# Performance work log

Measured on AMD Instinct MI355X. Metric: run time of the kernel, lower is better.

## Reference

```python
import jax, jax.numpy as jnp
import numpy as np

N, S, T, D = 8, 2048, 2048, 1024


def setup_inputs() -> dict:
    key0 = jax.random.key(0)
    ks = jax.random.split(key0, 6)
    scale = 1.0 / np.sqrt(D).astype(np.float32)
    query = jax.random.normal(ks[0], (N, S, D), dtype=jnp.float32)
    key = jax.random.normal(ks[1], (N, T, D), dtype=jnp.float32)
    value = jax.random.normal(ks[2], (N, T, D), dtype=jnp.float32)
    # nn.Linear(D, D, bias=False) weights, shape [out, in]
    Wq = jax.random.normal(ks[3], (D, D), dtype=jnp.float32) * scale
    Wk = jax.random.normal(ks[4], (D, D), dtype=jnp.float32) * scale
    Wv = jax.random.normal(ks[5], (D, D), dtype=jnp.float32) * scale
    # causal mask: 1 on/below diagonal, 0 above (zeros become -inf additively)
    attn_mask = jnp.tril(jnp.ones((S, T), dtype=jnp.float32))
    return {"key": key, "query": query, "value": value,
            "Wq": Wq, "Wk": Wk, "Wv": Wv, "attn_mask": attn_mask}


def reference(key, query, value, Wq, Wk, Wv, attn_mask):
    d = query.shape[-1]
    q = query @ Wq.T              # [N,S,D]
    k = key @ Wk.T                # [N,T,D]
    v = value @ Wv.T              # [N,T,D]
    scores = jnp.einsum('nsd,ntd->nst', q, k)          # [N,S,T]
    # masked_fill(mask==0, -inf) then ADD the (nonzero) mask values
    additive = jnp.where(attn_mask == 0, -jnp.inf, attn_mask)
    scores = scores + additive                          # broadcast [S,T] -> [N,S,T]
    # NOTE: torch code divides by D**(-0.5), i.e. multiplies by sqrt(D). Faithful.
    attn = jax.nn.softmax(scores * jnp.sqrt(jnp.float32(d)), axis=-1)
    return jnp.einsum('nst,ntd->nsd', attn, v)          # [N,S,D]
```

## Files before the change

kernel.cpp:

```cpp
#include <hip/hip_runtime.h>
#include <hip/hip_bf16.h>


typedef __attribute__((ext_vector_type(4))) float f32x4;
typedef __attribute__((ext_vector_type(8))) short bf16x8;
typedef __attribute__((ext_vector_type(4))) short s16x4;

#define DEVI __device__ __forceinline__

DEVI unsigned short f2bf(float x) {
  union { float f; unsigned u; } v; v.f = x;
  unsigned r = v.u + 0x7FFFu + ((v.u >> 16) & 1u);
  return (unsigned short)(r >> 16);
}
DEVI float bf2f(unsigned short b) {
  union { float f; unsigned u; } v; v.u = ((unsigned)b) << 16;
  return v.f;
}

DEVI void gload16(const void* g, void* l) {
#if __has_builtin(__builtin_amdgcn_global_load_lds)
  typedef __attribute__((address_space(1))) const unsigned int* gas_u32;
  typedef __attribute__((address_space(3))) unsigned int* las_u32;
  __builtin_amdgcn_global_load_lds(
      (gas_u32)(unsigned long long)g,
      (las_u32)(unsigned int)(unsigned long long)l, 16, 0, 0);
#else
  *(bf16x8*)l = *(const bf16x8*)g;
#endif
}

DEVI int xcd_swizzle(int bid, int nwg) {
  if (nwg & 7) return bid;
  int cpx = nwg >> 3;
  return (bid & 7) * cpx + (bid >> 3);
}

DEVI void stage_pair(const unsigned short* __restrict__ s0, long long rs0,
                     const unsigned short* __restrict__ s1, long long rs1,
                     short* lds, int tid) {
#pragma unroll
  for (int it = 0; it < 4; ++it) {
    int ii = it * 256 + tid;
    int r = ii >> 3;
    int c8 = (ii & 7) ^ (r & 7);
    const unsigned short* src = (c8 < 4)
        ? s0 + (long long)r * rs0 + (c8 & 3) * 8
        : s1 + (long long)r * rs1 + (c8 & 3) * 8;
    gload16(src, &lds[ii * 8]);
  }
}

constexpr int NB = 8, SS = 2048, TT = 2048, DD = 1024;
constexpr long long TILE_E = 16384;

__global__ __launch_bounds__(256) void split_hl_k(
    const float* __restrict__ in, unsigned short* __restrict__ hi,
    unsigned short* __restrict__ lo, long long n4)
{
  long long i = (long long)blockIdx.x * 256 + threadIdx.x;
  long long stride = (long long)gridDim.x * 256;
  for (; i < n4; i += stride) {
    f32x4 v = ((const f32x4*)in)[i];
    s16x4 h, l;
#pragma unroll
    for (int e = 0; e < 4; ++e) {
      unsigned short hh = f2bf(v[e]);
      h[e] = (short)hh;
      l[e] = (short)f2bf(v[e] - bf2f(hh));
    }
    ((s16x4*)hi)[i] = h;
    ((s16x4*)lo)[i] = l;
  }
}

__global__ __launch_bounds__(256) void split_h_k(
    const float* __restrict__ in, unsigned short* __restrict__ hi, long long n4)
{
  long long i = (long long)blockIdx.x * 256 + threadIdx.x;
  long long stride = (long long)gridDim.x * 256;
  for (; i < n4; i += stride) {
    f32x4 v = ((const f32x4*)in)[i];
    s16x4 h;
#pragma unroll
    for (int e = 0; e < 4; ++e) h[e] = (short)f2bf(v[e]);
    ((s16x4*)hi)[i] = h;
  }
}

template<int NMFMA, bool SPLIT_OUT>
__global__ __launch_bounds__(256, 2) void gemm_bt(
    const unsigned short* __restrict__ Ah_g, const unsigned short* __restrict__ Al_g,
    const unsigned short* __restrict__ Bh_g, const unsigned short* __restrict__ Bl_g,
    unsigned short* __restrict__ Chi, unsigned short* __restrict__ Clo,
    int Nn, int K,
    long long aStride, long long bStride, long long cStride,
    int tilesM, int tilesN)
{
  constexpr int NBUF = (NMFMA == 3) ? 4 : 2;
  __shared__ short lds[NBUF * 8192];

  int tid = threadIdx.x;
  int lane = tid & 63, wid = tid >> 6;
  int wr = wid >> 1, wc = wid & 1;
  int l15 = lane & 15, lq = lane >> 4;

  int wg = xcd_swizzle(blockIdx.x, gridDim.x);
  int tilesPer = tilesM * tilesN;
  int b = wg / tilesPer;
  int rem = wg % tilesPer;
  int mt = rem / tilesN, nt = rem % tilesN;

  const unsigned short* Agh = Ah_g + (long long)b * aStride + (long long)mt * 128 * K;
  const unsigned short* Bgh = Bh_g + (long long)b * bStride + (long long)nt * 128 * K;
  const unsigned short* Agl = (NMFMA == 3) ? Al_g + (long long)b * aStride + (long long)mt * 128 * K : nullptr;
  const unsigned short* Bgl = (NMFMA == 3) ? Bl_g + (long long)b * bStride + (long long)nt * 128 * K : nullptr;

  f32x4 acc[4][4];
#pragma unroll
  for (int i = 0; i < 4; ++i)
#pragma unroll
    for (int j = 0; j < 4; ++j) acc[i][j] = (f32x4){0.f, 0.f, 0.f, 0.f};

  auto stage = [&](int t, int half) {
    int k0 = t * 32;
    if constexpr (NMFMA == 3) {
      stage_pair(Agh + k0, K, Agl + k0, K, lds + half * 16384, tid);
      stage_pair(Bgh + k0, K, Bgl + k0, K, lds + half * 16384 + 8192, tid);
    } else {
      stage_pair(Agh + k0, K, Bgh + k0, K, lds + half * 8192, tid);
    }
  };

  auto compute = [&](int half) {
    if constexpr (NMFMA == 3) {
      const short* U = lds + half * 16384;
      const short* Vb2 = U + 8192;
      bf16x8 afh[4], afl[4], bfh[4], bfl[4];
#pragma unroll
      for (int i = 0; i < 4; ++i) {
        int ra = wr * 64 + i * 16 + l15;
        int sa = (ra & 7) << 4;
        afh[i] = *(const bf16x8*)(&U[((ra * 128 + lq * 16) ^ sa) >> 1]);
        afl[i] = *(const bf16x8*)(&U[((ra * 128 + 64 + lq * 16) ^ sa) >> 1]);
        int rb = wc * 64 + i * 16 + l15;
        int sb = (rb & 7) << 4;
        bfh[i] = *(const bf16x8*)(&Vb2[((rb * 128 + lq * 16) ^ sb) >> 1]);
        bfl[i] = *(const bf16x8*)(&Vb2[((rb * 128 + 64 + lq * 16) ^ sb) >> 1]);
      }
#pragma unroll
      for (int i = 0; i < 4; ++i)
#pragma unroll
        for (int j = 0; j < 4; ++j) {
          acc[i][j] = __builtin_amdgcn_mfma_f32_16x16x32_bf16(afh[i], bfh[j], acc[i][j], 0, 0, 0);
          acc[i][j] = __builtin_amdgcn_mfma_f32_16x16x32_bf16(afh[i], bfl[j], acc[i][j], 0, 0, 0);
          acc[i][j] = __builtin_amdgcn_mfma_f32_16x16x32_bf16(afl[i], bfh[j], acc[i][j], 0, 0, 0);
        }
    } else {
      const short* W = lds + half * 8192;
      bf16x8 af[4], bfr[4];
#pragma unroll
      for (int i = 0; i < 4; ++i) {
        int ra = wr * 64 + i * 16 + l15;
        af[i] = *(const bf16x8*)(&W[((ra * 128 + lq * 16) ^ ((ra & 7) << 4)) >> 1]);
        int rb = wc * 64 + i * 16 + l15;
        bfr[i] = *(const bf16x8*)(&W[((rb * 128 + 64 + lq * 16) ^ ((rb & 7) << 4)) >> 1]);
      }
#pragma unroll
      for (int i = 0; i < 4; ++i)
#pragma unroll
        for (int j = 0; j < 4; ++j)
          acc[i][j] = __builtin_amdgcn_mfma_f32_16x16x32_bf16(af[i], bfr[j], acc[i][j], 0, 0, 0);
    }
  };

  int NT = K >> 5;
  stage(0, 0);
  __syncthreads();
  for (int t = 0; t < NT; t += 2) {
    if (t + 1 < NT) stage(t + 1, 1);
    compute(0);
    __syncthreads();
    if (t + 2 < NT) stage(t + 2, 0);
    compute(1);
    __syncthreads();
  }

  unsigned short* ch = Chi + (long long)b * cStride;
  unsigned short* cl = SPLIT_OUT ? (Clo + (long long)b * cStride) : nullptr;
#pragma unroll
  for (int i = 0; i < 4; ++i)
#pragma unroll
    for (int j = 0; j < 4; ++j)
#pragma unroll
      for (int e = 0; e < 4; ++e) {
        int row = mt * 128 + wr * 64 + i * 16 + lq * 4 + e;
        int col = nt * 128 + wc * 64 + j * 16 + l15;
        float vv = acc[i][j][e];
        unsigned short h = f2bf(vv);
        ch[(long long)row * Nn + col] = h;
        if constexpr (SPLIT_OUT) cl[(long long)row * Nn + col] = f2bf(vv - bf2f(h));
      }
}

__global__ __launch_bounds__(256, 2) void qk_bt(
    const unsigned short* __restrict__ qh, const unsigned short* __restrict__ ql,
    const unsigned short* __restrict__ kh, const unsigned short* __restrict__ kl,
    float* __restrict__ Sg)
{
  __shared__ short lds[4 * 8192];

  int tid = threadIdx.x;
  int lane = tid & 63, wid = tid >> 6;
  int wr = wid >> 1, wc = wid & 1;
  int l15 = lane & 15, lq = lane >> 4;

  int wg = xcd_swizzle(blockIdx.x, gridDim.x);
  int b = wg / 136;
  int idx = wg % 136;
  int st = (int)((sqrtf(8.f * (float)idx + 1.f) - 1.f) * 0.5f);
  while ((st + 1) * (st + 2) / 2 <= idx) ++st;
  while (st * (st + 1) / 2 > idx) --st;
  int tt = idx - st * (st + 1) / 2;

  const unsigned short* Agh = qh + (long long)b * SS * DD + (long long)st * 128 * DD;
  const unsigned short* Agl = ql + (long long)b * SS * DD + (long long)st * 128 * DD;
  const unsigned short* Bgh = kh + (long long)b * TT * DD + (long long)tt * 128 * DD;
  const unsigned short* Bgl = kl + (long long)b * TT * DD + (long long)tt * 128 * DD;

  f32x4 acc[4][4];
#pragma unroll
  for (int i = 0; i < 4; ++i)
#pragma unroll
    for (int j = 0; j < 4; ++j) acc[i][j] = (f32x4){0.f, 0.f, 0.f, 0.f};

  auto stage = [&](int t, int half) {
    int k0 = t * 32;
    stage_pair(Agh + k0, DD, Agl + k0, DD, lds + half * 16384, tid);
    stage_pair(Bgh + k0, DD, Bgl + k0, DD, lds + half * 16384 + 8192, tid);
  };
  auto compute = [&](int half) {
    const short* U = lds + half * 16384;
    const short* Vb2 = U + 8192;
    bf16x8 afh[4], afl[4], bfh[4], bfl[4];
#pragma unroll
    for (int i = 0; i < 4; ++i) {
      int ra = wr * 64 + i * 16 + l15;
      int sa = (ra & 7) << 4;
      afh[i] = *(const bf16x8*)(&U[((ra * 128 + lq * 16) ^ sa) >> 1]);
      afl[i] = *(const bf16x8*)(&U[((ra * 128 + 64 + lq * 16) ^ sa) >> 1]);
      int rb = wc * 64 + i * 16 + l15;
      int sb = (rb & 7) << 4;
      bfh[i] = *(const bf16x8*)(&Vb2[((rb * 128 + lq * 16) ^ sb) >> 1]);
      bfl[i] = *(const bf16x8*)(&Vb2[((rb * 128 + 64 + lq * 16) ^ sb) >> 1]);
    }
#pragma unroll
    for (int i = 0; i < 4; ++i)
#pragma unroll
      for (int j = 0; j < 4; ++j) {
        acc[i][j] = __builtin_amdgcn_mfma_f32_16x16x32_bf16(afh[i], bfh[j], acc[i][j], 0, 0, 0);
        acc[i][j] = __builtin_amdgcn_mfma_f32_16x16x32_bf16(afh[i], bfl[j], acc[i][j], 0, 0, 0);
        acc[i][j] = __builtin_amdgcn_mfma_f32_16x16x32_bf16(afl[i], bfh[j], acc[i][j], 0, 0, 0);
      }
  };

  stage(0, 0);
  __syncthreads();
  for (int t = 0; t < 32; t += 2) {
    if (t + 1 < 32) stage(t + 1, 1);
    compute(0);
    __syncthreads();
    if (t + 2 < 32) stage(t + 2, 0);
    compute(1);
    __syncthreads();
  }

  float* Sb = Sg + ((long long)b * 136 + idx) * TILE_E;
#pragma unroll
  for (int i = 0; i < 4; ++i)
#pragma unroll
    for (int j = 0; j < 4; ++j)
#pragma unroll
      for (int e = 0; e < 4; ++e) {
        int row = wr * 64 + i * 16 + lq * 4 + e;
        int col = wc * 64 + j * 16 + l15;
        Sb[(long long)row * 128 + col] = acc[i][j][e];
      }
}

__global__ __launch_bounds__(256) void softmax_kernel(float* __restrict__ Sg)
{
  __shared__ float red[8];
  int blk = blockIdx.x;
  int b = blk >> 11, s = blk & 2047;
  int st = s >> 7, r = s & 127;
  long long tri = (long long)st * (st + 1) / 2;
  const float* tb = Sg + ((long long)b * 136 + tri) * TILE_E + (long long)r * 128;

  int tid = threadIdx.x;
  int lane = tid & 63, wid = tid >> 6;

  int c0 = tid * 8;
  int tt = c0 >> 7, cc = c0 & 127;
  bool live = (c0 <= s);
  f32x4 v0 = {0.f, 0.f, 0.f, 0.f}, v1 = {0.f, 0.f, 0.f, 0.f};
  if (live) {
    const float* seg = tb + (long long)tt * TILE_E + cc;
    v0 = *(const f32x4*)seg;
    v1 = *(const f32x4*)(seg + 4);
  }

  float m = -3.0e38f;
#pragma unroll
  for (int e = 0; e < 4; ++e) {
    if (c0 + e <= s) m = fmaxf(m, v0[e]);
    if (c0 + 4 + e <= s) m = fmaxf(m, v1[e]);
  }
#pragma unroll
  for (int o = 32; o > 0; o >>= 1) m = fmaxf(m, __shfl_xor(m, o));
  if (lane == 0) red[wid] = m;
  __syncthreads();
  m = fmaxf(fmaxf(red[0], red[1]), fmaxf(red[2], red[3]));

  const float C = 46.16624130844683f;
  float p0[4], p1[4];
  float sum = 0.f;
#pragma unroll
  for (int e = 0; e < 4; ++e) {
    p0[e] = (c0 + e <= s) ? exp2f((v0[e] - m) * C) : 0.f;
    sum += p0[e];
    p1[e] = (c0 + 4 + e <= s) ? exp2f((v1[e] - m) * C) : 0.f;
    sum += p1[e];
  }
#pragma unroll
  for (int o = 32; o > 0; o >>= 1) sum += __shfl_xor(sum, o);
  if (lane == 0) red[4 + wid] = sum;
  __syncthreads();
  float inv = 1.f / (red[4] + red[5] + red[6] + red[7]);

  union { bf16x8 v; s16x4 h[2]; } w;
#pragma unroll
  for (int e = 0; e < 4; ++e) {
    w.h[0][e] = (short)f2bf(p0[e] * inv);
    w.h[1][e] = (short)f2bf(p1[e] * inv);
  }
  __syncthreads();
  if (c0 < (st + 1) * 128) {
    unsigned short* pw = (unsigned short*)Sg +
        (((long long)b * 136 + tri + tt) * TILE_E) * 2 + (long long)r * 256 + cc;
    *(bf16x8*)pw = w.v;
  }
}

__global__ __launch_bounds__(256, 2) void pv_bt(
    const unsigned short* __restrict__ P, const unsigned short* __restrict__ vT,
    float* __restrict__ Out)
{
  __shared__ short lds[2 * 8192];

  int tid = threadIdx.x;
  int lane = tid & 63, wid = tid >> 6;
  int wr = wid >> 1, wc = wid & 1;
  int l15 = lane & 15, lq = lane >> 4;

  int wg = xcd_swizzle(blockIdx.x, gridDim.x);
  int b = wg >> 7;
  int rem = wg & 127;
  int st = rem >> 3, dt = rem & 7;

  const unsigned short* Ps = P + ((long long)b * 136 + (long long)st * (st + 1) / 2) * (TILE_E * 2);
  const unsigned short* Vb = vT + (long long)b * DD * TT + (long long)dt * 128 * TT;
  int NT = (st + 1) * 4;

  f32x4 acc[4][4];
#pragma unroll
  for (int i = 0; i < 4; ++i)
#pragma unroll
    for (int j = 0; j < 4; ++j) acc[i][j] = (f32x4){0.f, 0.f, 0.f, 0.f};

  auto stage = [&](int t, int half) {
    int t0 = t * 32;
    const unsigned short* s0 = Ps + (long long)(t0 >> 7) * (TILE_E * 2) + (t0 & 127);
    stage_pair(s0, 256, Vb + t0, TT, lds + half * 8192, tid);
  };
  auto compute = [&](int half) {
    const short* W = lds + half * 8192;
    bf16x8 af[4], bfr[4];
#pragma unroll
    for (int i = 0; i < 4; ++i) {
      int ra = wr * 64 + i * 16 + l15;
      af[i] = *(const bf16x8*)(&W[((ra * 128 + lq * 16) ^ ((ra & 7) << 4)) >> 1]);
      int rb = wc * 64 + i * 16 + l15;
      bfr[i] = *(const bf16x8*)(&W[((rb * 128 + 64 + lq * 16) ^ ((rb & 7) << 4)) >> 1]);
    }
#pragma unroll
    for (int i = 0; i < 4; ++i)
#pragma unroll
      for (int j = 0; j < 4; ++j)
        acc[i][j] = __builtin_amdgcn_mfma_f32_16x16x32_bf16(af[i], bfr[j], acc[i][j], 0, 0, 0);
  };

  stage(0, 0);
  __syncthreads();
  for (int t = 0; t < NT; t += 2) {
    if (t + 1 < NT) stage(t + 1, 1);
    compute(0);
    __syncthreads();
    if (t + 2 < NT) stage(t + 2, 0);
    compute(1);
    __syncthreads();
  }

  float* Ob = Out + (long long)b * SS * DD;
#pragma unroll
  for (int i = 0; i < 4; ++i)
#pragma unroll
    for (int j = 0; j < 4; ++j)
#pragma unroll
      for (int e = 0; e < 4; ++e) {
        int row = st * 128 + wr * 64 + i * 16 + lq * 4 + e;
        int col = dt * 128 + wc * 64 + j * 16 + l15;
        Ob[(long long)row * DD + col] = acc[i][j][e];
      }
}

extern "C" void kernel_launch(void* const* d_in, const int* in_sizes, int n_in,
                              void* d_out, int out_size, void* d_ws, size_t ws_size,
                              hipStream_t stream) {
  (void)in_sizes; (void)n_in; (void)out_size;
  const float* key   = (const float*)d_in[0];
  const float* query = (const float*)d_in[1];
  const float* value = (const float*)d_in[2];
  const float* Wq    = (const float*)d_in[3];
  const float* Wk    = (const float*)d_in[4];
  const float* Wv    = (const float*)d_in[5];
  float* Out = (float*)d_out;

  const long long SD = (long long)SS * DD;
  const long long DT = (long long)DD * TT;
  const long long WN = (long long)DD * DD;

  const unsigned long long PLANE_B  = (unsigned long long)SD * 2;
  const unsigned long long WPLANE_B = (unsigned long long)WN * 2;
  const unsigned long long SCORE_B  = 136ull * TILE_E * 4;

  auto need = [&](int g) -> unsigned long long {
    return 5ull * WPLANE_B + (unsigned long long)g * (SCORE_B + 5ull * PLANE_B);
  };
  int G = 1;
  for (int g : {8, 4, 2, 1}) if (ws_size >= need(g)) { G = g; break; }

  char* ws = (char*)d_ws;
  size_t off = 0;
  auto alloc = [&](unsigned long long bytes) { char* p = ws + off; off += bytes; return p; };

  unsigned short* wqh = (unsigned short*)alloc(WPLANE_B);
  unsigned short* wql = (unsigned short*)alloc(WPLANE_B);
  unsigned short* wkh = (unsigned short*)alloc(WPLANE_B);
  unsigned short* wkl = (unsigned short*)alloc(WPLANE_B);
  unsigned short* wvh = (unsigned short*)alloc(WPLANE_B);
  char* slab = alloc((unsigned long long)G * SCORE_B);
  unsigned short* qh  = (unsigned short*)alloc((unsigned long long)G * PLANE_B);
  unsigned short* ql  = (unsigned short*)alloc((unsigned long long)G * PLANE_B);
  unsigned short* kh  = (unsigned short*)alloc((unsigned long long)G * PLANE_B);
  unsigned short* kl  = (unsigned short*)alloc((unsigned long long)G * PLANE_B);
  unsigned short* vT  = (unsigned short*)alloc((unsigned long long)G * PLANE_B);

  unsigned short* iah = (unsigned short*)slab;
  unsigned short* ial = (unsigned short*)(slab + (unsigned long long)G * PLANE_B);
  float* Sg = (float*)slab;

  split_hl_k<<<512, 256, 0, stream>>>(Wq, wqh, wql, WN / 4);
  split_hl_k<<<512, 256, 0, stream>>>(Wk, wkh, wkl, WN / 4);
  split_h_k<<<512, 256, 0, stream>>>(Wv, wvh, WN / 4);

  for (int b0 = 0; b0 < NB; b0 += G) {
    long long n4 = (long long)G * SD / 4;
    split_hl_k<<<2048, 256, 0, stream>>>(query + (long long)b0 * SD, iah, ial, n4);
    gemm_bt<3, true><<<G * 128, 256, 0, stream>>>(
        iah, ial, wqh, wql, qh, ql, DD, DD, SD, 0, SD, 16, 8);
    split_hl_k<<<2048, 256, 0, stream>>>(key + (long long)b0 * SD, iah, ial, n4);
    gemm_bt<3, true><<<G * 128, 256, 0, stream>>>(
        iah, ial, wkh, wkl, kh, kl, DD, DD, SD, 0, SD, 16, 8);
    split_h_k<<<2048, 256, 0, stream>>>(value + (long long)b0 * SD, iah, n4);
    gemm_bt<1, false><<<G * 128, 256, 0, stream>>>(
        wvh, nullptr, iah, nullptr, vT, nullptr, TT, DD, 0, SD, DT, 8, 16);
    qk_bt<<<G * 136, 256, 0, stream>>>(qh, ql, kh, kl, Sg);
    softmax_kernel<<<G * SS, 256, 0, stream>>>(Sg);
    pv_bt<<<G * 128, 256, 0, stream>>>(
        (const unsigned short*)Sg, vT, Out + (long long)b0 * SD);
  }
}
```

Baseline: 530.0 us.

## Retile causal QK^T kernel to 64x128 tiles with two-wave blocks and single buffer

The QK^T kernel now uses 64-row by 128-column tiles computed by 128-thread blocks (two waves), doubling the grid to 272 tiles per batch with a new triangular index mapping over half-height row strips. Staging becomes single-buffered with inline swizzled global-to-LDS loads, and MFMA sections are bracketed with s_setprio. The aim is more blocks and occupancy to fill CUs and better load balance on the causal triangle. In exchange it loses the double-buffered overlap of loads and compute and gets less operand reuse per tile.

```diff
diff --git a/kernel.cpp b/kernel.cpp
--- a/kernel.cpp
+++ b/kernel.cpp
@@ -203,30 +203,30 @@
       }
 }
 
-__global__ __launch_bounds__(256, 2) void qk_bt(
+__global__ __launch_bounds__(128, 3) void qk_bt(
     const unsigned short* __restrict__ qh, const unsigned short* __restrict__ ql,
     const unsigned short* __restrict__ kh, const unsigned short* __restrict__ kl,
     float* __restrict__ Sg)
 {
-  __shared__ short lds[4 * 8192];
+  __shared__ short lds[12288];
+  short* Ab = lds;
+  short* Bb = lds + 4096;
 
   int tid = threadIdx.x;
   int lane = tid & 63, wid = tid >> 6;
-  int wr = wid >> 1, wc = wid & 1;
   int l15 = lane & 15, lq = lane >> 4;
 
   int wg = xcd_swizzle(blockIdx.x, gridDim.x);
-  int b = wg / 136;
-  int idx = wg % 136;
-  int st = (int)((sqrtf(8.f * (float)idx + 1.f) - 1.f) * 0.5f);
-  while ((st + 1) * (st + 2) / 2 <= idx) ++st;
-  while (st * (st + 1) / 2 > idx) --st;
-  int tt = idx - st * (st + 1) / 2;
-
-  const unsigned short* Agh = qh + (long long)b * SS * DD + (long long)st * 128 * DD;
-  const unsigned short* Agl = ql + (long long)b * SS * DD + (long long)st * 128 * DD;
-  const unsigned short* Bgh = kh + (long long)b * TT * DD + (long long)tt * 128 * DD;
-  const unsigned short* Bgl = kl + (long long)b * TT * DD + (long long)tt * 128 * DD;
+  int b = wg / 272;
+  int idx = wg % 272;
+  int st = 0, cum = 0;
+  while (cum + (st >> 1) + 1 <= idx) { cum += (st >> 1) + 1; ++st; }
+  int tc = idx - cum;
+
+  const unsigned short* Agh = qh + (long long)b * SS * DD + (long long)st * 64 * DD;
+  const unsigned short* Agl = ql + (long long)b * SS * DD + (long long)st * 64 * DD;
+  const unsigned short* Bgh = kh + (long long)b * TT * DD + (long long)tc * 128 * DD;
+  const unsigned short* Bgl = kl + (long long)b * TT * DD + (long long)tc * 128 * DD;
 
   f32x4 acc[4][4];
 #pragma unroll
@@ -234,25 +234,43 @@
 #pragma unroll
     for (int j = 0; j < 4; ++j) acc[i][j] = (f32x4){0.f, 0.f, 0.f, 0.f};
 
-  auto stage = [&](int t, int half) {
+  for (int t = 0; t < 32; ++t) {
     int k0 = t * 32;
-    stage_pair(Agh + k0, DD, Agl + k0, DD, lds + half * 16384, tid);
-    stage_pair(Bgh + k0, DD, Bgl + k0, DD, lds + half * 16384 + 8192, tid);
-  };
-  auto compute = [&](int half) {
-    const short* U = lds + half * 16384;
-    const short* Vb2 = U + 8192;
+    __syncthreads();
+#pragma unroll
+    for (int it = 0; it < 4; ++it) {
+      int ii = it * 128 + tid;
+      int r = ii >> 3;
+      int c8 = (ii & 7) ^ (r & 7);
+      const unsigned short* src = (c8 < 4)
+          ? Agh + (long long)r * DD + k0 + (c8 & 3) * 8
+          : Agl + (long long)r * DD + k0 + (c8 & 3) * 8;
+      gload16(src, &Ab[ii * 8]);
+    }
+#pragma unroll
+    for (int it = 0; it < 8; ++it) {
+      int ii = it * 128 + tid;
+      int r = ii >> 3;
+      int c8 = (ii & 7) ^ (r & 7);
+      const unsigned short* src = (c8 < 4)
+          ? Bgh + (long long)r * DD + k0 + (c8 & 3) * 8
+          : Bgl + (long long)r * DD + k0 + (c8 & 3) * 8;
+      gload16(src, &Bb[ii * 8]);
+    }
+    __syncthreads();
+
+    __builtin_amdgcn_s_setprio(1);
     bf16x8 afh[4], afl[4], bfh[4], bfl[4];
 #pragma unroll
     for (int i = 0; i < 4; ++i) {
-      int ra = wr * 64 + i * 16 + l15;
+      int ra = i * 16 + l15;
       int sa = (ra & 7) << 4;
-      afh[i] = *(const bf16x8*)(&U[((ra * 128 + lq * 16) ^ sa) >> 1]);
-      afl[i] = *(const bf16x8*)(&U[((ra * 128 + 64 + lq * 16) ^ sa) >> 1]);
-      int rb = wc * 64 + i * 16 + l15;
+      afh[i] = *(const bf16x8*)(&Ab[((ra * 128 + lq * 16) ^ sa) >> 1]);
+      afl[i] = *(const bf16x8*)(&Ab[((ra * 128 + 64 + lq * 16) ^ sa) >> 1]);
+      int rb = wid * 64 + i * 16 + l15;
       int sb = (rb & 7) << 4;
-      bfh[i] = *(const bf16x8*)(&Vb2[((rb * 128 + lq * 16) ^ sb) >> 1]);
-      bfl[i] = *(const bf16x8*)(&Vb2[((rb * 128 + 64 + lq * 16) ^ sb) >> 1]);
+      bfh[i] = *(const bf16x8*)(&Bb[((rb * 128 + lq * 16) ^ sb) >> 1]);
+      bfl[i] = *(const bf16x8*)(&Bb[((rb * 128 + 64 + lq * 16) ^ sb) >> 1]);
     }
 #pragma unroll
     for (int i = 0; i < 4; ++i)
@@ -262,28 +280,20 @@
         acc[i][j] = __builtin_amdgcn_mfma_f32_16x16x32_bf16(afh[i], bfl[j], acc[i][j], 0, 0, 0);
         acc[i][j] = __builtin_amdgcn_mfma_f32_16x16x32_bf16(afl[i], bfh[j], acc[i][j], 0, 0, 0);
       }
-  };
-
-  stage(0, 0);
-  __syncthreads();
-  for (int t = 0; t < 32; t += 2) {
-    if (t + 1 < 32) stage(t + 1, 1);
-    compute(0);
-    __syncthreads();
-    if (t + 2 < 32) stage(t + 2, 0);
-    compute(1);
-    __syncthreads();
-  }
-
-  float* Sb = Sg + ((long long)b * 136 + idx) * TILE_E;
+    __builtin_amdgcn_s_setprio(0);
+  }
+
+  int st128 = st >> 1;
+  long long ptile = (long long)b * 136 + (long long)st128 * (st128 + 1) / 2 + tc;
+  float* Sb = Sg + ptile * TILE_E + (long long)(st & 1) * 64 * 128;
 #pragma unroll
   for (int i = 0; i < 4; ++i)
 #pragma unroll
     for (int j = 0; j < 4; ++j)
 #pragma unroll
       for (int e = 0; e < 4; ++e) {
-        int row = wr * 64 + i * 16 + lq * 4 + e;
-        int col = wc * 64 + j * 16 + l15;
+        int row = i * 16 + lq * 4 + e;
+        int col = wid * 64 + j * 16 + l15;
         Sb[(long long)row * 128 + col] = acc[i][j][e];
       }
 }
@@ -485,7 +495,7 @@
     split_h_k<<<2048, 256, 0, stream>>>(value + (long long)b0 * SD, iah, n4);
     gemm_bt<1, false><<<G * 128, 256, 0, stream>>>(
         wvh, nullptr, iah, nullptr, vT, nullptr, TT, DD, 0, SD, DT, 8, 16);
-    qk_bt<<<G * 136, 256, 0, stream>>>(qh, ql, kh, kl, Sg);
+    qk_bt<<<G * 272, 128, 0, stream>>>(qh, ql, kh, kl, Sg);
     softmax_kernel<<<G * SS, 256, 0, stream>>>(Sg);
     pv_bt<<<G * 128, 256, 0, stream>>>(
         (const unsigned short*)Sg, vT, Out + (long long)b0 * SD);
```

Measured after the change: 655.1 us. +23.6%, slower.

## Prefetch two stages ahead with vmcnt waits, persistent two-tile GEMM, reverse PV order

Applied to the files above, without the earlier changes.

Replaces the double-buffered __syncthreads loop with a scheme that issues two stages up front, waits on vmcnt counts plus a raw barrier, and refills the buffer just consumed. This keeps one global load in flight during each compute step. Compute sections run at raised wave priority. The projection GEMM now processes two M tiles per workgroup with half the grid, and the PV kernel schedules long causal rows first for better load balance. The hand-written waitcnt values depend on the exact number of loads per stage, which makes them fragile.

```diff
diff --git a/kernel.cpp b/kernel.cpp
--- a/kernel.cpp
+++ b/kernel.cpp
@@ -36,6 +36,9 @@
   return (bid & 7) * cpx + (bid >> 3);
 }
 
+#define WAITBAR(N) asm volatile("s_waitcnt vmcnt(" #N ")\ns_barrier" ::: "memory")
+#define BAR()      asm volatile("s_barrier" ::: "memory")
+
 DEVI void stage_pair(const unsigned short* __restrict__ s0, long long rs0,
                      const unsigned short* __restrict__ s1, long long rs1,
                      short* lds, int tid) {
@@ -97,8 +100,8 @@
     long long aStride, long long bStride, long long cStride,
     int tilesM, int tilesN)
 {
-  constexpr int NBUF = (NMFMA == 3) ? 4 : 2;
-  __shared__ short lds[NBUF * 8192];
+  constexpr int HALF = (NMFMA == 3) ? 16384 : 8192;
+  __shared__ short lds[2 * HALF];
 
   int tid = threadIdx.x;
   int lane = tid & 63, wid = tid >> 6;
@@ -106,101 +109,110 @@
   int l15 = lane & 15, lq = lane >> 4;
 
   int wg = xcd_swizzle(blockIdx.x, gridDim.x);
-  int tilesPer = tilesM * tilesN;
+  int tilesM2 = tilesM >> 1;
+  int tilesPer = tilesM2 * tilesN;
   int b = wg / tilesPer;
   int rem = wg % tilesPer;
-  int mt = rem / tilesN, nt = rem % tilesN;
-
-  const unsigned short* Agh = Ah_g + (long long)b * aStride + (long long)mt * 128 * K;
+  int mt2 = rem / tilesN, nt = rem % tilesN;
+
   const unsigned short* Bgh = Bh_g + (long long)b * bStride + (long long)nt * 128 * K;
-  const unsigned short* Agl = (NMFMA == 3) ? Al_g + (long long)b * aStride + (long long)mt * 128 * K : nullptr;
   const unsigned short* Bgl = (NMFMA == 3) ? Bl_g + (long long)b * bStride + (long long)nt * 128 * K : nullptr;
 
-  f32x4 acc[4][4];
-#pragma unroll
-  for (int i = 0; i < 4; ++i)
-#pragma unroll
-    for (int j = 0; j < 4; ++j) acc[i][j] = (f32x4){0.f, 0.f, 0.f, 0.f};
-
-  auto stage = [&](int t, int half) {
-    int k0 = t * 32;
-    if constexpr (NMFMA == 3) {
-      stage_pair(Agh + k0, K, Agl + k0, K, lds + half * 16384, tid);
-      stage_pair(Bgh + k0, K, Bgl + k0, K, lds + half * 16384 + 8192, tid);
-    } else {
-      stage_pair(Agh + k0, K, Bgh + k0, K, lds + half * 8192, tid);
+  for (int hm = 0; hm < 2; ++hm) {
+    int mt = mt2 + hm * tilesM2;
+    const unsigned short* Agh = Ah_g + (long long)b * aStride + (long long)mt * 128 * K;
+    const unsigned short* Agl = (NMFMA == 3) ? Al_g + (long long)b * aStride + (long long)mt * 128 * K : nullptr;
+
+    f32x4 acc[4][4];
+#pragma unroll
+    for (int i = 0; i < 4; ++i)
+#pragma unroll
+      for (int j = 0; j < 4; ++j) acc[i][j] = (f32x4){0.f, 0.f, 0.f, 0.f};
+
+    auto stage = [&](int t, int h) {
+      int k0 = t * 32;
+      if constexpr (NMFMA == 3) {
+        stage_pair(Agh + k0, K, Agl + k0, K, lds + h * HALF, tid);
+        stage_pair(Bgh + k0, K, Bgl + k0, K, lds + h * HALF + 8192, tid);
+      } else {
+        stage_pair(Agh + k0, K, Bgh + k0, K, lds + h * HALF, tid);
+      }
+    };
+    auto compute = [&](int h) {
+      __builtin_amdgcn_s_setprio(1);
+      if constexpr (NMFMA == 3) {
+        const short* U = lds + h * HALF;
+        const short* V = U + 8192;
+        bf16x8 afh[4], afl[4], bfh[4], bfl[4];
+#pragma unroll
+        for (int i = 0; i < 4; ++i) {
+          int ra = wr * 64 + i * 16 + l15;
+          int sa = (ra & 7) << 4;
+          afh[i] = *(const bf16x8*)(&U[((ra * 128 + lq * 16) ^ sa) >> 1]);
+          afl[i] = *(const bf16x8*)(&U[((ra * 128 + 64 + lq * 16) ^ sa) >> 1]);
+          int rb = wc * 64 + i * 16 + l15;
+          int sb = (rb & 7) << 4;
+          bfh[i] = *(const bf16x8*)(&V[((rb * 128 + lq * 16) ^ sb) >> 1]);
+          bfl[i] = *(const bf16x8*)(&V[((rb * 128 + 64 + lq * 16) ^ sb) >> 1]);
+        }
+#pragma unroll
+        for (int i = 0; i < 4; ++i)
+#pragma unroll
+          for (int j = 0; j < 4; ++j) {
+            acc[i][j] = __builtin_amdgcn_mfma_f32_16x16x32_bf16(afh[i], bfh[j], acc[i][j], 0, 0, 0);
+            acc[i][j] = __builtin_amdgcn_mfma_f32_16x16x32_bf16(afh[i], bfl[j], acc[i][j], 0, 0, 0);
+            acc[i][j] = __builtin_amdgcn_mfma_f32_16x16x32_bf16(afl[i], bfh[j], acc[i][j], 0, 0, 0);
+          }
+      } else {
+        const short* W = lds + h * HALF;
+        bf16x8 af[4], bfr[4];
+#pragma unroll
+        for (int i = 0; i < 4; ++i) {
+          int ra = wr * 64 + i * 16 + l15;
+          af[i] = *(const bf16x8*)(&W[((ra * 128 + lq * 16) ^ ((ra & 7) << 4)) >> 1]);
+          int rb = wc * 64 + i * 16 + l15;
+          bfr[i] = *(const bf16x8*)(&W[((rb * 128 + 64 + lq * 16) ^ ((rb & 7) << 4)) >> 1]);
+        }
+#pragma unroll
+        for (int i = 0; i < 4; ++i)
+#pragma unroll
+          for (int j = 0; j < 4; ++j)
+            acc[i][j] = __builtin_amdgcn_mfma_f32_16x16x32_bf16(af[i], bfr[j], acc[i][j], 0, 0, 0);
+      }
+      __builtin_amdgcn_s_setprio(0);
+    };
+
+    int NT = K >> 5;
+    stage(0, 0);
+    stage(1, 1);
+    for (int t = 0; t < NT; ++t) {
+      if (t < NT - 1) {
+        if constexpr (NMFMA == 3) WAITBAR(8); else WAITBAR(4);
+      } else {
+        WAITBAR(0);
+      }
+      compute(t & 1);
+      BAR();
+      if (t + 2 < NT) stage(t + 2, t & 1);
     }
-  };
-
-  auto compute = [&](int half) {
-    if constexpr (NMFMA == 3) {
-      const short* U = lds + half * 16384;
-      const short* Vb2 = U + 8192;
-      bf16x8 afh[4], afl[4], bfh[4], bfl[4];
-#pragma unroll
-      for (int i = 0; i < 4; ++i) {
-        int ra = wr * 64 + i * 16 + l15;
-        int sa = (ra & 7) << 4;
-        afh[i] = *(const bf16x8*)(&U[((ra * 128 + lq * 16) ^ sa) >> 1]);
-        afl[i] = *(const bf16x8*)(&U[((ra * 128 + 64 + lq * 16) ^ sa) >> 1]);
-        int rb = wc * 64 + i * 16 + l15;
-        int sb = (rb & 7) << 4;
-        bfh[i] = *(const bf16x8*)(&Vb2[((rb * 128 + lq * 16) ^ sb) >> 1]);
-        bfl[i] = *(const bf16x8*)(&Vb2[((rb * 128 + 64 + lq * 16) ^ sb) >> 1]);
-      }
-#pragma unroll
-      for (int i = 0; i < 4; ++i)
-#pragma unroll
-        for (int j = 0; j < 4; ++j) {
-          acc[i][j] = __builtin_amdgcn_mfma_f32_16x16x32_bf16(afh[i], bfh[j], acc[i][j], 0, 0, 0);
-          acc[i][j] = __builtin_amdgcn_mfma_f32_16x16x32_bf16(afh[i], bfl[j], acc[i][j], 0, 0, 0);
-          acc[i][j] = __builtin_amdgcn_mfma_f32_16x16x32_bf16(afl[i], bfh[j], acc[i][j], 0, 0, 0);
+
+    unsigned short* ch = Chi + (long long)b * cStride;
+    unsigned short* cl = SPLIT_OUT ? (Clo + (long long)b * cStride) : nullptr;
+#pragma unroll
+    for (int i = 0; i < 4; ++i)
+#pragma unroll
+      for (int j = 0; j < 4; ++j)
+#pragma unroll
+        for (int e = 0; e < 4; ++e) {
+          int row = mt * 128 + wr * 64 + i * 16 + lq * 4 + e;
+          int col = nt * 128 + wc * 64 + j * 16 + l15;
+          float vv = acc[i][j][e];
+          unsigned short h = f2bf(vv);
+          ch[(long long)row * Nn + col] = h;
+          if constexpr (SPLIT_OUT) cl[(long long)row * Nn + col] = f2bf(vv - bf2f(h));
         }
-    } else {
-      const short* W = lds + half * 8192;
-      bf16x8 af[4], bfr[4];
-#pragma unroll
-      for (int i = 0; i < 4; ++i) {
-        int ra = wr * 64 + i * 16 + l15;
-        af[i] = *(const bf16x8*)(&W[((ra * 128 + lq * 16) ^ ((ra & 7) << 4)) >> 1]);
-        int rb = wc * 64 + i * 16 + l15;
-        bfr[i] = *(const bf16x8*)(&W[((rb * 128 + 64 + lq * 16) ^ ((rb & 7) << 4)) >> 1]);
-      }
-#pragma unroll
-      for (int i = 0; i < 4; ++i)
-#pragma unroll
-        for (int j = 0; j < 4; ++j)
-          acc[i][j] = __builtin_amdgcn_mfma_f32_16x16x32_bf16(af[i], bfr[j], acc[i][j], 0, 0, 0);
-    }
-  };
-
-  int NT = K >> 5;
-  stage(0, 0);
-  __syncthreads();
-  for (int t = 0; t < NT; t += 2) {
-    if (t + 1 < NT) stage(t + 1, 1);
-    compute(0);
-    __syncthreads();
-    if (t + 2 < NT) stage(t + 2, 0);
-    compute(1);
-    __syncthreads();
-  }
-
-  unsigned short* ch = Chi + (long long)b * cStride;
-  unsigned short* cl = SPLIT_OUT ? (Clo + (long long)b * cStride) : nullptr;
-#pragma unroll
-  for (int i = 0; i < 4; ++i)
-#pragma unroll
-    for (int j = 0; j < 4; ++j)
-#pragma unroll
-      for (int e = 0; e < 4; ++e) {
-        int row = mt * 128 + wr * 64 + i * 16 + lq * 4 + e;
-        int col = nt * 128 + wc * 64 + j * 16 + l15;
-        float vv = acc[i][j][e];
-        unsigned short h = f2bf(vv);
-        ch[(long long)row * Nn + col] = h;
-        if constexpr (SPLIT_OUT) cl[(long long)row * Nn + col] = f2bf(vv - bf2f(h));
-      }
+    BAR();
+  }
 }
 
 __global__ __launch_bounds__(256, 2) void qk_bt(
@@ -208,7 +220,7 @@
     const unsigned short* __restrict__ kh, const unsigned short* __restrict__ kl,
     float* __restrict__ Sg)
 {
-  __shared__ short lds[4 * 8192];
+  __shared__ short lds[2 * 16384];
 
   int tid = threadIdx.x;
   int lane = tid & 63, wid = tid >> 6;
@@ -234,14 +246,15 @@
 #pragma unroll
     for (int j = 0; j < 4; ++j) acc[i][j] = (f32x4){0.f, 0.f, 0.f, 0.f};
 
-  auto stage = [&](int t, int half) {
+  auto stage = [&](int t, int h) {
     int k0 = t * 32;
-    stage_pair(Agh + k0, DD, Agl + k0, DD, lds + half * 16384, tid);
-    stage_pair(Bgh + k0, DD, Bgl + k0, DD, lds + half * 16384 + 8192, tid);
+    stage_pair(Agh + k0, DD, Agl + k0, DD, lds + h * 16384, tid);
+    stage_pair(Bgh + k0, DD, Bgl + k0, DD, lds + h * 16384 + 8192, tid);
   };
-  auto compute = [&](int half) {
-    const short* U = lds + half * 16384;
-    const short* Vb2 = U + 8192;
+  auto compute = [&](int h) {
+    __builtin_amdgcn_s_setprio(1);
+    const short* U = lds + h * 16384;
+    const short* V = U + 8192;
     bf16x8 afh[4], afl[4], bfh[4], bfl[4];
 #pragma unroll
     for (int i = 0; i < 4; ++i) {
@@ -251,8 +264,8 @@
       afl[i] = *(const bf16x8*)(&U[((ra * 128 + 64 + lq * 16) ^ sa) >> 1]);
       int rb = wc * 64 + i * 16 + l15;
       int sb = (rb & 7) << 4;
-      bfh[i] = *(const bf16x8*)(&Vb2[((rb * 128 + lq * 16) ^ sb) >> 1]);
-      bfl[i] = *(const bf16x8*)(&Vb2[((rb * 128 + 64 + lq * 16) ^ sb) >> 1]);
+      bfh[i] = *(const bf16x8*)(&V[((rb * 128 + lq * 16) ^ sb) >> 1]);
+      bfl[i] = *(const bf16x8*)(&V[((rb * 128 + 64 + lq * 16) ^ sb) >> 1]);
     }
 #pragma unroll
     for (int i = 0; i < 4; ++i)
@@ -262,17 +275,16 @@
         acc[i][j] = __builtin_amdgcn_mfma_f32_16x16x32_bf16(afh[i], bfl[j], acc[i][j], 0, 0, 0);
         acc[i][j] = __builtin_amdgcn_mfma_f32_16x16x32_bf16(afl[i], bfh[j], acc[i][j], 0, 0, 0);
       }
+    __builtin_amdgcn_s_setprio(0);
   };
 
   stage(0, 0);
-  __syncthreads();
-  for (int t = 0; t < 32; t += 2) {
-    if (t + 1 < 32) stage(t + 1, 1);
-    compute(0);
-    __syncthreads();
-    if (t + 2 < 32) stage(t + 2, 0);
-    compute(1);
-    __syncthreads();
+  stage(1, 1);
+  for (int t = 0; t < 32; ++t) {
+    if (t < 31) WAITBAR(8); else WAITBAR(0);
+    compute(t & 1);
+    BAR();
+    if (t + 2 < 32) stage(t + 2, t & 1);
   }
 
   float* Sb = Sg + ((long long)b * 136 + idx) * TILE_E;
@@ -366,7 +378,8 @@
   int wg = xcd_swizzle(blockIdx.x, gridDim.x);
   int b = wg >> 7;
   int rem = wg & 127;
-  int st = rem >> 3, dt = rem & 7;
+  int st = 15 - (rem >> 3);
+  int dt = rem & 7;
 
   const unsigned short* Ps = P + ((long long)b * 136 + (long long)st * (st + 1) / 2) * (TILE_E * 2);
   const unsigned short* Vb = vT + (long long)b * DD * TT + (long long)dt * 128 * TT;
@@ -378,13 +391,14 @@
 #pragma unroll
     for (int j = 0; j < 4; ++j) acc[i][j] = (f32x4){0.f, 0.f, 0.f, 0.f};
 
-  auto stage = [&](int t, int half) {
+  auto stage = [&](int t, int h) {
     int t0 = t * 32;
     const unsigned short* s0 = Ps + (long long)(t0 >> 7) * (TILE_E * 2) + (t0 & 127);
-    stage_pair(s0, 256, Vb + t0, TT, lds + half * 8192, tid);
+    stage_pair(s0, 256, Vb + t0, TT, lds + h * 8192, tid);
   };
-  auto compute = [&](int half) {
-    const short* W = lds + half * 8192;
+  auto compute = [&](int h) {
+    __builtin_amdgcn_s_setprio(1);
+    const short* W = lds + h * 8192;
     bf16x8 af[4], bfr[4];
 #pragma unroll
     for (int i = 0; i < 4; ++i) {
@@ -398,17 +412,16 @@
 #pragma unroll
       for (int j = 0; j < 4; ++j)
         acc[i][j] = __builtin_amdgcn_mfma_f32_16x16x32_bf16(af[i], bfr[j], acc[i][j], 0, 0, 0);
+    __builtin_amdgcn_s_setprio(0);
   };
 
   stage(0, 0);
-  __syncthreads();
-  for (int t = 0; t < NT; t += 2) {
-    if (t + 1 < NT) stage(t + 1, 1);
-    compute(0);
-    __syncthreads();
-    if (t + 2 < NT) stage(t + 2, 0);
-    compute(1);
-    __syncthreads();
+  stage(1, 1);
+  for (int t = 0; t < NT; ++t) {
+    if (t < NT - 1) WAITBAR(4); else WAITBAR(0);
+    compute(t & 1);
+    BAR();
+    if (t + 2 < NT) stage(t + 2, t & 1);
   }
 
   float* Ob = Out + (long long)b * SS * DD;
@@ -477,13 +490,13 @@
   for (int b0 = 0; b0 < NB; b0 += G) {
     long long n4 = (long long)G * SD / 4;
     split_hl_k<<<2048, 256, 0, stream>>>(query + (long long)b0 * SD, iah, ial, n4);
-    gemm_bt<3, true><<<G * 128, 256, 0, stream>>>(
+    gemm_bt<3, true><<<G * 64, 256, 0, stream>>>(
         iah, ial, wqh, wql, qh, ql, DD, DD, SD, 0, SD, 16, 8);
     split_hl_k<<<2048, 256, 0, stream>>>(key + (long long)b0 * SD, iah, ial, n4);
-    gemm_bt<3, true><<<G * 128, 256, 0, stream>>>(
+    gemm_bt<3, true><<<G * 64, 256, 0, stream>>>(
         iah, ial, wkh, wkl, kh, kl, DD, DD, SD, 0, SD, 16, 8);
     split_h_k<<<2048, 256, 0, stream>>>(value + (long long)b0 * SD, iah, n4);
-    gemm_bt<1, false><<<G * 128, 256, 0, stream>>>(
+    gemm_bt<1, false><<<G * 64, 256, 0, stream>>>(
         wvh, nullptr, iah, nullptr, vT, nullptr, TT, DD, 0, SD, DT, 8, 16);
     qk_bt<<<G * 136, 256, 0, stream>>>(qh, ql, kh, kl, Sg);
     softmax_kernel<<<G * SS, 256, 0, stream>>>(Sg);
```

Measured after the change: 538.8 us. No clear change (+1.7%).
